# Kernel optimization log

Measured on AMD Instinct MI355X. Metric: run time of the kernel, lower is better.

## Reference

```python
import jax, jax.numpy as jnp
import numpy as np

D_IN = 1024
D_OUT = 1024
NUM_HEADS = 16
HEAD_DIM = D_OUT // NUM_HEADS


def setup_inputs() -> dict:
    key = jax.random.key(0)
    ks = jax.random.split(key, 4)
    B, T = 2, 2048
    x = jax.random.normal(ks[0], (B, T, D_IN), dtype=jnp.float32)
    # Linear(d_in, 3*d_out, bias=False): weight shape (3*d_out, d_in)
    w_qkv = jax.random.normal(ks[1], (3 * D_OUT, D_IN), dtype=jnp.float32) * (1.0 / np.sqrt(D_IN))
    # Linear(d_out, d_out) with bias
    w_out = jax.random.normal(ks[2], (D_OUT, D_OUT), dtype=jnp.float32) * (1.0 / np.sqrt(D_OUT))
    b_out = jax.random.normal(ks[3], (D_OUT,), dtype=jnp.float32) * 0.01
    return {"x": x, "w_qkv": w_qkv, "w_out": w_out, "b_out": b_out}


def reference(x, w_qkv, w_out, b_out):
    B, T, C = x.shape
    H, Dh = NUM_HEADS, HEAD_DIM
    qkv = jnp.einsum('btc,fc->btf', x, w_qkv)          # (B, T, 3*d_out)
    q, k, v = jnp.split(qkv, 3, axis=-1)
    # (B, H, T, Dh)
    q = q.reshape(B, T, H, Dh).transpose(0, 2, 1, 3)
    k = k.reshape(B, T, H, Dh).transpose(0, 2, 1, 3)
    v = v.reshape(B, T, H, Dh).transpose(0, 2, 1, 3)
    scale = 1.0 / np.sqrt(Dh).astype(np.float32)
    scores = jnp.einsum('bhqd,bhkd->bhqk', q, k) * scale
    causal = jnp.tril(jnp.ones((T, T), dtype=bool))    # True = keep
    scores = jnp.where(causal, scores, -jnp.inf)
    weights = jax.nn.softmax(scores, axis=-1)
    y = jnp.einsum('bhqk,bhkd->bhqd', weights, v)
    y = y.transpose(0, 2, 1, 3).reshape(B, T, C)
    return jnp.einsum('btc,oc->bto', y, w_out) + b_out
```

## Files before the change

kernel.cpp:

```cpp
#include <hip/hip_runtime.h>
#include <stdint.h>


typedef __bf16 bf16x8 __attribute__((ext_vector_type(8)));
typedef float  f32x4  __attribute__((ext_vector_type(4)));
typedef float  f32x16 __attribute__((ext_vector_type(16)));

#define MFMA16(a, b, c) __builtin_amdgcn_mfma_f32_16x16x32_bf16((a), (b), (c), 0, 0, 0)
#define MFMA32(a, b, c) __builtin_amdgcn_mfma_f32_32x32x16_bf16((a), (b), (c), 0, 0, 0)

__device__ __forceinline__ unsigned short f2bf(float f) {
    union { float f; unsigned int u; } c;
    c.f = f;
    unsigned int u = c.u;
    return (unsigned short)((u + 0x7fffu + ((u >> 16) & 1u)) >> 16);
}

__device__ __forceinline__ unsigned cvtpk(float lo, float hi) {
    unsigned r;
    asm("v_cvt_pk_bf16_f32 %0, %1, %2" : "=v"(r) : "v"(lo), "v"(hi));
    return r;
}

__global__ __launch_bounds__(256) void cvt3_kernel(const float* __restrict__ a,
                                                   const float* __restrict__ b,
                                                   const float* __restrict__ c,
                                                   unsigned short* __restrict__ out,
                                                   int na4, int nb4, int ntot4) {
    int i = blockIdx.x * 256 + threadIdx.x;
    const int stride = gridDim.x * 256;
    for (; i < ntot4; i += stride) {
        const float4* src;
        int j;
        if (i < na4)            { src = (const float4*)a; j = i; }
        else if (i < na4 + nb4) { src = (const float4*)b; j = i - na4; }
        else                    { src = (const float4*)c; j = i - na4 - nb4; }
        float4 v = src[j];
        ushort4 o;
        o.x = f2bf(v.x); o.y = f2bf(v.y); o.z = f2bf(v.z); o.w = f2bf(v.w);
        reinterpret_cast<ushort4*>(out)[i] = o;
    }
}

__device__ __forceinline__ void gload_lds16(const void* g, void* l) {
    __builtin_amdgcn_global_load_lds((const __attribute__((address_space(1))) void*)g,
                                     (__attribute__((address_space(3))) void*)l,
                                     16, 0, 0);
}

__device__ __forceinline__ void gemm_core_128(const unsigned short* __restrict__ A,
                                              const unsigned short* __restrict__ B,
                                              int K, int tM, int tN,
                                              unsigned short* As, unsigned short* Bs,
                                              f32x4 acc[4][4]) {
    const int tid  = threadIdx.x;
    const int lane = tid & 63;
    const int w    = tid >> 6;
    const int wr   = w >> 1, wc = w & 1;
    const int lr   = lane & 15, lg = lane >> 4;

    const int o0 = tid * 16;
    const int o1 = o0 + 4096;
    const int row0 = o0 >> 6, cb0 = o0 & 63;
    const int row1 = o1 >> 6, cb1 = o1 & 63;

    const char* Ab = (const char*)A;
    const char* Bb = (const char*)B;
    const size_t rstride = (size_t)K * 2;

    for (int kt = 0; kt < K; kt += 32) {
        const size_t kbyte = (size_t)kt * 2;
        gload_lds16(Ab + (size_t)(tM + row0) * rstride + kbyte + cb0, (char*)As + o0);
        gload_lds16(Ab + (size_t)(tM + row1) * rstride + kbyte + cb1, (char*)As + o1);
        gload_lds16(Bb + (size_t)(tN + row0) * rstride + kbyte + cb0, (char*)Bs + o0);
        gload_lds16(Bb + (size_t)(tN + row1) * rstride + kbyte + cb1, (char*)Bs + o1);
        __syncthreads();

        bf16x8 a[4], b[4];
#pragma unroll
        for (int m = 0; m < 4; ++m)
            a[m] = *reinterpret_cast<const bf16x8*>(As + (wr * 64 + m * 16 + lr) * 32 + lg * 8);
#pragma unroll
        for (int n = 0; n < 4; ++n)
            b[n] = *reinterpret_cast<const bf16x8*>(Bs + (wc * 64 + n * 16 + lr) * 32 + lg * 8);
#pragma unroll
        for (int m = 0; m < 4; ++m)
#pragma unroll
            for (int n = 0; n < 4; ++n)
                acc[m][n] = MFMA16(a[m], b[n], acc[m][n]);
        __syncthreads();
    }
}

__global__ __launch_bounds__(256) void gemm_qkv_kernel(const unsigned short* __restrict__ Xb,
                                                       const unsigned short* __restrict__ Wb,
                                                       unsigned short* __restrict__ Qo,
                                                       unsigned short* __restrict__ Ko,
                                                       unsigned short* __restrict__ Vt) {
    __shared__ __align__(16) unsigned short As[128 * 32];
    __shared__ __align__(16) unsigned short Bs[128 * 32];
    f32x4 acc[4][4];
#pragma unroll
    for (int m = 0; m < 4; ++m)
#pragma unroll
        for (int n = 0; n < 4; ++n)
#pragma unroll
            for (int r = 0; r < 4; ++r) acc[m][n][r] = 0.0f;

    const int wg = (blockIdx.x & 7) * 96 + (blockIdx.x >> 3);
    const int tM = (wg / 24) * 128;
    const int tN = (wg % 24) * 128;
    gemm_core_128(Xb, Wb, 1024, tM, tN, As, Bs, acc);

    const int lane = threadIdx.x & 63, w = threadIdx.x >> 6;
    const int wr = w >> 1, wc = w & 1, lr = lane & 15, lg = lane >> 4;
    const float QSCALE = 0.125f * 1.44269504088896340736f;
#pragma unroll
    for (int m = 0; m < 4; ++m)
#pragma unroll
        for (int n = 0; n < 4; ++n)
#pragma unroll
            for (int r = 0; r < 4; ++r) {
                const int gr = tM + wr * 64 + m * 16 + 4 * lg + r;
                const int gc = tN + wc * 64 + n * 16 + lr;
                const float v = acc[m][n][r];
                const int bb = gr >> 11, t = gr & 2047;
                const int kind = gc >> 10, c = gc & 1023;
                const int h = c >> 6, d = c & 63;
                const int bh = bb * 16 + h;
                if (kind == 0) {
                    Qo[((size_t)bh * 2048 + t) * 64 + d] = f2bf(v * QSCALE);
                } else if (kind == 1) {
                    const int off = ((t >> 5) << 11) + ((d >> 4) << 9) + ((t & 31) << 4) + (d & 15);
                    Ko[((size_t)bh << 17) + off] = f2bf(v);
                } else {
                    const int off = ((t >> 6) << 12) + ((d >> 5) << 11) + (((t >> 4) & 3) << 9)
                                  + ((d & 31) << 4) + (t & 15);
                    Vt[((size_t)bh << 17) + off] = f2bf(v);
                }
            }
}

__global__ __launch_bounds__(256) void gemm_out_kernel(const unsigned short* __restrict__ Yb,
                                                       const unsigned short* __restrict__ Wob,
                                                       const float* __restrict__ bias,
                                                       float* __restrict__ out) {
    __shared__ __align__(16) unsigned short As[128 * 32];
    __shared__ __align__(16) unsigned short Bs[64 * 32];
    const int tid = threadIdx.x, lane = tid & 63, w = tid >> 6;
    const int wr = w >> 1, wc = w & 1, lr = lane & 15, lg = lane >> 4;

    const int wg = (blockIdx.x & 7) * 64 + (blockIdx.x >> 3);
    const int tM = (wg >> 4) * 128;
    const int tN = (wg & 15) * 64;

    f32x4 acc[4][2];
#pragma unroll
    for (int m = 0; m < 4; ++m)
#pragma unroll
        for (int n = 0; n < 2; ++n)
#pragma unroll
            for (int r = 0; r < 4; ++r) acc[m][n][r] = 0.0f;

    const int o0 = tid * 16;
    const int o1 = o0 + 4096;
    const int rowA0 = o0 >> 6, cbA0 = o0 & 63;
    const int rowA1 = o1 >> 6, cbA1 = o1 & 63;
    const int rowB  = o0 >> 6, cbB  = o0 & 63;

    const char* Ab = (const char*)Yb;
    const char* Bb = (const char*)Wob;

    for (int kt = 0; kt < 1024; kt += 32) {
        const size_t kbyte = (size_t)kt * 2;
        gload_lds16(Ab + (size_t)(tM + rowA0) * 2048 + kbyte + cbA0, (char*)As + o0);
        gload_lds16(Ab + (size_t)(tM + rowA1) * 2048 + kbyte + cbA1, (char*)As + o1);
        gload_lds16(Bb + (size_t)(tN + rowB) * 2048 + kbyte + cbB, (char*)Bs + o0);
        __syncthreads();

        bf16x8 a[4], b[2];
#pragma unroll
        for (int m = 0; m < 4; ++m)
            a[m] = *reinterpret_cast<const bf16x8*>(As + (wr * 64 + m * 16 + lr) * 32 + lg * 8);
#pragma unroll
        for (int n = 0; n < 2; ++n)
            b[n] = *reinterpret_cast<const bf16x8*>(Bs + (wc * 32 + n * 16 + lr) * 32 + lg * 8);
#pragma unroll
        for (int m = 0; m < 4; ++m)
#pragma unroll
            for (int n = 0; n < 2; ++n)
                acc[m][n] = MFMA16(a[m], b[n], acc[m][n]);
        __syncthreads();
    }

#pragma unroll
    for (int m = 0; m < 4; ++m)
#pragma unroll
        for (int n = 0; n < 2; ++n)
#pragma unroll
            for (int r = 0; r < 4; ++r) {
                const int gr = tM + wr * 64 + m * 16 + 4 * lg + r;
                const int gc = tN + wc * 32 + n * 16 + lr;
                out[(size_t)gr * 1024 + gc] = acc[m][n][r] + bias[gc];
            }
}

__global__ __launch_bounds__(256, 2) void attn_kernel(const unsigned short* __restrict__ Q,
                                                      const unsigned short* __restrict__ Kb,
                                                      const unsigned short* __restrict__ Vt,
                                                      unsigned short* __restrict__ Y) {
    __shared__ __align__(16) float4 part[3][64][9];
    const int tid = threadIdx.x, lane = tid & 63, w = tid >> 6;
    const int l31 = lane & 31, hi = lane >> 5;
    const int fo  = (l31 << 4) + (hi << 3);

    const int bid = blockIdx.x;
    const int wg  = (bid & 7) * 256 + (bid >> 3);
    const int bh  = wg >> 6;
    const int qt  = 63 - (wg & 63);
    const int qw  = qt * 32;

    const unsigned short* Qh = Q  + (size_t)bh * 2048 * 64;
    const unsigned short* Kh = Kb + ((size_t)bh << 17);
    const unsigned short* Vh = Vt + ((size_t)bh << 17);

    bf16x8 qf[4];
#pragma unroll
    for (int c = 0; c < 4; ++c)
        qf[c] = *reinterpret_cast<const bf16x8*>(Qh + (size_t)(qw + l31) * 64 + c * 16 + hi * 8);

    f32x16 o0, o1;
#pragma unroll
    for (int r = 0; r < 16; ++r) { o0[r] = 0.0f; o1[r] = 0.0f; }
    float lrun = 0.0f;

    const int qg  = qw + l31;
    const int n64 = (qw >> 6) + 1;

    union UB { unsigned u[4]; bf16x8 v; };
#define PACK_HALF(SV, base, OUT) {                                        \
        unsigned lo01 = cvtpk(SV[(base) + 0], SV[(base) + 1]);            \
        unsigned lo23 = cvtpk(SV[(base) + 2], SV[(base) + 3]);            \
        unsigned hi01 = cvtpk(SV[(base) + 4], SV[(base) + 5]);            \
        unsigned hi23 = cvtpk(SV[(base) + 6], SV[(base) + 7]);            \
        unsigned s01  = hi ? lo01 : hi01;                                 \
        unsigned s23  = hi ? lo23 : hi23;                                 \
        unsigned r01  = __shfl_xor(s01, 32, 64);                          \
        unsigned r23  = __shfl_xor(s23, 32, 64);                          \
        OUT.u[0] = hi ? r01  : lo01;                                      \
        OUT.u[1] = hi ? r23  : lo23;                                      \
        OUT.u[2] = hi ? hi01 : r01;                                       \
        OUT.u[3] = hi ? hi23 : r23; }

    for (int j = w; j < n64; j += 4) {
        const int kb = j << 6;
        const bool act1 = (kb + 32 <= qw + 31);

        const unsigned short* Kt = Kh + ((size_t)(kb >> 5) << 11);
        const unsigned short* Vb = Vh + ((size_t)(kb >> 6) << 12);
        bf16x8 kf0[4], kf1[4], vf0[4], vf1[4];
#pragma unroll
        for (int c = 0; c < 4; ++c)
            kf0[c] = *reinterpret_cast<const bf16x8*>(Kt + (c << 9) + fo);
        if (act1) {
#pragma unroll
            for (int c = 0; c < 4; ++c)
                kf1[c] = *reinterpret_cast<const bf16x8*>(Kt + 2048 + (c << 9) + fo);
        }
#pragma unroll
        for (int c = 0; c < 4; ++c) {
            vf0[c] = *reinterpret_cast<const bf16x8*>(Vb + (c << 9) + fo);
            vf1[c] = *reinterpret_cast<const bf16x8*>(Vb + 2048 + (c << 9) + fo);
        }

        f32x16 s0, s1;
#pragma unroll
        for (int r = 0; r < 16; ++r) { s0[r] = 0.0f; s1[r] = 0.0f; }
#pragma unroll
        for (int c = 0; c < 4; ++c) s0 = MFMA32(kf0[c], qf[c], s0);
        if (act1) {
#pragma unroll
            for (int c = 0; c < 4; ++c) s1 = MFMA32(kf1[c], qf[c], s1);
        }

        if (kb + 31 > qw) {
#pragma unroll
            for (int r = 0; r < 16; ++r) {
                const int kv = kb + (r & 3) + 8 * (r >> 2) + 4 * hi;
                s0[r] = (kv > qg) ? -INFINITY : s0[r];
            }
        }
        if (kb + 63 > qw) {
#pragma unroll
            for (int r = 0; r < 16; ++r) {
                const int kv = kb + 32 + (r & 3) + 8 * (r >> 2) + 4 * hi;
                s1[r] = (kv > qg) ? -INFINITY : s1[r];
            }
        }

#pragma unroll
        for (int r = 0; r < 16; ++r) {
            s0[r] = __builtin_amdgcn_exp2f(s0[r]);
            s1[r] = __builtin_amdgcn_exp2f(s1[r]);
        }

        float u8[8];
#pragma unroll
        for (int r = 0; r < 8; ++r)
            u8[r] = (s0[r] + s0[r + 8]) + (s1[r] + s1[r + 8]);
        float us = ((u8[0] + u8[1]) + (u8[2] + u8[3])) + ((u8[4] + u8[5]) + (u8[6] + u8[7]));
        us += __shfl_xor(us, 32, 64);
        lrun += us;

        UB p0, p1, p2, p3;
        PACK_HALF(s0, 0, p0); PACK_HALF(s0, 8, p1);
        PACK_HALF(s1, 0, p2); PACK_HALF(s1, 8, p3);

        o0 = MFMA32(vf0[0], p0.v, o0);
        o0 = MFMA32(vf0[1], p1.v, o0);
        o0 = MFMA32(vf0[2], p2.v, o0);
        o0 = MFMA32(vf0[3], p3.v, o0);
        o1 = MFMA32(vf1[0], p0.v, o1);
        o1 = MFMA32(vf1[1], p1.v, o1);
        o1 = MFMA32(vf1[2], p2.v, o1);
        o1 = MFMA32(vf1[3], p3.v, o1);
    }
#undef PACK_HALF

    if (w) {
        float4* row = &part[w - 1][lane][0];
#pragma unroll
        for (int q4 = 0; q4 < 4; ++q4)
            row[q4] = make_float4(o0[q4 * 4], o0[q4 * 4 + 1], o0[q4 * 4 + 2], o0[q4 * 4 + 3]);
#pragma unroll
        for (int q4 = 0; q4 < 4; ++q4)
            row[4 + q4] = make_float4(o1[q4 * 4], o1[q4 * 4 + 1], o1[q4 * 4 + 2], o1[q4 * 4 + 3]);
        row[8] = make_float4(lrun, 0.0f, 0.0f, 0.0f);
    }
    __syncthreads();
    if (w == 0) {
#pragma unroll
        for (int wv = 0; wv < 3; ++wv) {
            const float4* row = &part[wv][lane][0];
#pragma unroll
            for (int q4 = 0; q4 < 4; ++q4) {
                float4 a = row[q4], b = row[4 + q4];
                o0[q4 * 4] += a.x; o0[q4 * 4 + 1] += a.y; o0[q4 * 4 + 2] += a.z; o0[q4 * 4 + 3] += a.w;
                o1[q4 * 4] += b.x; o1[q4 * 4 + 1] += b.y; o1[q4 * 4 + 2] += b.z; o1[q4 * 4 + 3] += b.w;
            }
            lrun += row[8].x;
        }

        const float inv = 1.0f / lrun;
        const int bb = bh >> 4, hh = bh & 15;
        unsigned short* Yrow = Y + ((size_t)(bb * 2048 + qg)) * 1024 + hh * 64;
#pragma unroll
        for (int r = 0; r < 16; ++r) {
            const int d = (r & 3) + 8 * (r >> 2) + 4 * hi;
            Yrow[d]      = f2bf(o0[r] * inv);
            Yrow[32 + d] = f2bf(o1[r] * inv);
        }
    }
}

extern "C" void kernel_launch(void* const* d_in, const int* in_sizes, int n_in,
                              void* d_out, int out_size, void* d_ws, size_t ws_size,
                              hipStream_t stream) {
    (void)in_sizes; (void)n_in; (void)out_size; (void)ws_size;
    const float* x     = (const float*)d_in[0];
    const float* w_qkv = (const float*)d_in[1];
    const float* w_out = (const float*)d_in[2];
    const float* b_out = (const float*)d_in[3];
    float* out = (float*)d_out;

    unsigned short* xb    = (unsigned short*)d_ws;
    unsigned short* Yb    = xb;
    unsigned short* wqkvb = xb    + (size_t)4096 * 1024;
    unsigned short* woutb = wqkvb + (size_t)3072 * 1024;
    unsigned short* Qb    = woutb + (size_t)1024 * 1024;
    unsigned short* Kbuf  = Qb    + (size_t)32 * 2048 * 64;
    unsigned short* Vt    = Kbuf  + (size_t)32 * 2048 * 64;

    const int na4 = 4096 * 1024 / 4, nb4 = 3072 * 1024 / 4, nc4 = 1024 * 1024 / 4;
    cvt3_kernel<<<2048, 256, 0, stream>>>(x, w_qkv, w_out, xb, na4, nb4, na4 + nb4 + nc4);
    gemm_qkv_kernel<<<768, 256, 0, stream>>>(xb, wqkvb, Qb, Kbuf, Vt);
    attn_kernel<<<2048, 256, 0, stream>>>(Qb, Kbuf, Vt, Yb);
    gemm_out_kernel<<<512, 256, 0, stream>>>(Yb, woutb, b_out, out);
}
```

Before: 172.0 us.

## Triple-buffer LDS staging in QKV and output projection GEMMs

Replaces the single-buffered load/sync/compute loops in both projection GEMMs with a 3-stage ring of LDS buffers. Loads for tile i+2 are issued while tile i is computed, and a partial vmcnt wait plus one barrier per iteration replace the two __syncthreads. This is meant to hide global-load latency behind MFMA work. In exchange it triples LDS use per block, which could reduce occupancy, and it relies on hand-written waitcnt counts staying correct.

```diff
diff --git a/kernel.cpp b/kernel.cpp
--- a/kernel.cpp
+++ b/kernel.cpp
@@ -48,72 +48,69 @@
                                      16, 0, 0);
 }
 
-__device__ __forceinline__ void gemm_core_128(const unsigned short* __restrict__ A,
-                                              const unsigned short* __restrict__ B,
-                                              int K, int tM, int tN,
-                                              unsigned short* As, unsigned short* Bs,
-                                              f32x4 acc[4][4]) {
-    const int tid  = threadIdx.x;
-    const int lane = tid & 63;
-    const int w    = tid >> 6;
-    const int wr   = w >> 1, wc = w & 1;
-    const int lr   = lane & 15, lg = lane >> 4;
-
-    const int o0 = tid * 16;
-    const int o1 = o0 + 4096;
-    const int row0 = o0 >> 6, cb0 = o0 & 63;
-    const int row1 = o1 >> 6, cb1 = o1 & 63;
-
-    const char* Ab = (const char*)A;
-    const char* Bb = (const char*)B;
-    const size_t rstride = (size_t)K * 2;
-
-    for (int kt = 0; kt < K; kt += 32) {
-        const size_t kbyte = (size_t)kt * 2;
-        gload_lds16(Ab + (size_t)(tM + row0) * rstride + kbyte + cb0, (char*)As + o0);
-        gload_lds16(Ab + (size_t)(tM + row1) * rstride + kbyte + cb1, (char*)As + o1);
-        gload_lds16(Bb + (size_t)(tN + row0) * rstride + kbyte + cb0, (char*)Bs + o0);
-        gload_lds16(Bb + (size_t)(tN + row1) * rstride + kbyte + cb1, (char*)Bs + o1);
-        __syncthreads();
-
-        bf16x8 a[4], b[4];
-#pragma unroll
-        for (int m = 0; m < 4; ++m)
-            a[m] = *reinterpret_cast<const bf16x8*>(As + (wr * 64 + m * 16 + lr) * 32 + lg * 8);
-#pragma unroll
-        for (int n = 0; n < 4; ++n)
-            b[n] = *reinterpret_cast<const bf16x8*>(Bs + (wc * 64 + n * 16 + lr) * 32 + lg * 8);
-#pragma unroll
-        for (int m = 0; m < 4; ++m)
-#pragma unroll
-            for (int n = 0; n < 4; ++n)
-                acc[m][n] = MFMA16(a[m], b[n], acc[m][n]);
-        __syncthreads();
-    }
-}
-
 __global__ __launch_bounds__(256) void gemm_qkv_kernel(const unsigned short* __restrict__ Xb,
                                                        const unsigned short* __restrict__ Wb,
                                                        unsigned short* __restrict__ Qo,
                                                        unsigned short* __restrict__ Ko,
                                                        unsigned short* __restrict__ Vt) {
-    __shared__ __align__(16) unsigned short As[128 * 32];
-    __shared__ __align__(16) unsigned short Bs[128 * 32];
-    f32x4 acc[4][4];
-#pragma unroll
-    for (int m = 0; m < 4; ++m)
-#pragma unroll
-        for (int n = 0; n < 4; ++n)
-#pragma unroll
-            for (int r = 0; r < 4; ++r) acc[m][n][r] = 0.0f;
+    __shared__ __align__(16) unsigned short As[3 * 4096];
+    __shared__ __align__(16) unsigned short Bs[3 * 4096];
+    const int tid = threadIdx.x, lane = tid & 63, w = tid >> 6;
+    const int wr = w >> 1, wc = w & 1, lr = lane & 15, lg = lane >> 4;
 
     const int wg = (blockIdx.x & 7) * 96 + (blockIdx.x >> 3);
     const int tM = (wg / 24) * 128;
     const int tN = (wg % 24) * 128;
-    gemm_core_128(Xb, Wb, 1024, tM, tN, As, Bs, acc);
-
-    const int lane = threadIdx.x & 63, w = threadIdx.x >> 6;
-    const int wr = w >> 1, wc = w & 1, lr = lane & 15, lg = lane >> 4;
+
+    f32x4 acc[4][4];
+#pragma unroll
+    for (int m = 0; m < 4; ++m)
+#pragma unroll
+        for (int n = 0; n < 4; ++n)
+#pragma unroll
+            for (int r = 0; r < 4; ++r) acc[m][n][r] = 0.0f;
+
+    const int o0 = tid * 16, o1 = o0 + 4096;
+    const int row0 = o0 >> 6, cb0 = o0 & 63;
+    const int row1 = o1 >> 6, cb1 = o1 & 63;
+    const char* Ab = (const char*)Xb;
+    const char* Bb = (const char*)Wb;
+
+#define STAGE_Q(bi, kt) { const size_t kb_ = (size_t)(kt) * 2;                                 \
+        gload_lds16(Ab + (size_t)(tM + row0) * 2048 + kb_ + cb0, (char*)As + (bi) * 8192 + o0); \
+        gload_lds16(Ab + (size_t)(tM + row1) * 2048 + kb_ + cb1, (char*)As + (bi) * 8192 + o1); \
+        gload_lds16(Bb + (size_t)(tN + row0) * 2048 + kb_ + cb0, (char*)Bs + (bi) * 8192 + o0); \
+        gload_lds16(Bb + (size_t)(tN + row1) * 2048 + kb_ + cb1, (char*)Bs + (bi) * 8192 + o1); }
+
+    STAGE_Q(0, 0);
+    STAGE_Q(1, 32);
+    for (int i = 0; i < 32; ++i) {
+        __builtin_amdgcn_sched_barrier(0);
+        if (i < 31) asm volatile("s_waitcnt vmcnt(4) lgkmcnt(0)" ::: "memory");
+        else        asm volatile("s_waitcnt vmcnt(0) lgkmcnt(0)" ::: "memory");
+        __builtin_amdgcn_sched_barrier(0);
+        __builtin_amdgcn_s_barrier();
+        __builtin_amdgcn_sched_barrier(0);
+        const int bi = i % 3;
+        if (i + 2 < 32) STAGE_Q((i + 2) % 3, (i + 2) * 32);
+
+        const unsigned short* Av = As + bi * 4096;
+        const unsigned short* Bv = Bs + bi * 4096;
+        bf16x8 a[4], b[4];
+#pragma unroll
+        for (int m = 0; m < 4; ++m)
+            a[m] = *reinterpret_cast<const bf16x8*>(Av + (wr * 64 + m * 16 + lr) * 32 + lg * 8);
+#pragma unroll
+        for (int n = 0; n < 4; ++n)
+            b[n] = *reinterpret_cast<const bf16x8*>(Bv + (wc * 64 + n * 16 + lr) * 32 + lg * 8);
+#pragma unroll
+        for (int m = 0; m < 4; ++m)
+#pragma unroll
+            for (int n = 0; n < 4; ++n)
+                acc[m][n] = MFMA16(a[m], b[n], acc[m][n]);
+    }
+#undef STAGE_Q
+
     const float QSCALE = 0.125f * 1.44269504088896340736f;
 #pragma unroll
     for (int m = 0; m < 4; ++m)
@@ -145,8 +142,8 @@
                                                        const unsigned short* __restrict__ Wob,
                                                        const float* __restrict__ bias,
                                                        float* __restrict__ out) {
-    __shared__ __align__(16) unsigned short As[128 * 32];
-    __shared__ __align__(16) unsigned short Bs[64 * 32];
+    __shared__ __align__(16) unsigned short As[3 * 4096];
+    __shared__ __align__(16) unsigned short Bs[3 * 2048];
     const int tid = threadIdx.x, lane = tid & 63, w = tid >> 6;
     const int wr = w >> 1, wc = w & 1, lr = lane & 15, lg = lane >> 4;
 
@@ -162,36 +159,46 @@
 #pragma unroll
             for (int r = 0; r < 4; ++r) acc[m][n][r] = 0.0f;
 
-    const int o0 = tid * 16;
-    const int o1 = o0 + 4096;
+    const int o0 = tid * 16, o1 = o0 + 4096;
     const int rowA0 = o0 >> 6, cbA0 = o0 & 63;
     const int rowA1 = o1 >> 6, cbA1 = o1 & 63;
-    const int rowB  = o0 >> 6, cbB  = o0 & 63;
-
+    const int rowB = o0 >> 6, cbB = o0 & 63;
     const char* Ab = (const char*)Yb;
     const char* Bb = (const char*)Wob;
 
-    for (int kt = 0; kt < 1024; kt += 32) {
-        const size_t kbyte = (size_t)kt * 2;
-        gload_lds16(Ab + (size_t)(tM + rowA0) * 2048 + kbyte + cbA0, (char*)As + o0);
-        gload_lds16(Ab + (size_t)(tM + rowA1) * 2048 + kbyte + cbA1, (char*)As + o1);
-        gload_lds16(Bb + (size_t)(tN + rowB) * 2048 + kbyte + cbB, (char*)Bs + o0);
-        __syncthreads();
-
+#define STAGE_O(bi, kt) { const size_t kb_ = (size_t)(kt) * 2;                                   \
+        gload_lds16(Ab + (size_t)(tM + rowA0) * 2048 + kb_ + cbA0, (char*)As + (bi) * 8192 + o0); \
+        gload_lds16(Ab + (size_t)(tM + rowA1) * 2048 + kb_ + cbA1, (char*)As + (bi) * 8192 + o1); \
+        gload_lds16(Bb + (size_t)(tN + rowB) * 2048 + kb_ + cbB, (char*)Bs + (bi) * 4096 + o0); }
+
+    STAGE_O(0, 0);
+    STAGE_O(1, 32);
+    for (int i = 0; i < 32; ++i) {
+        __builtin_amdgcn_sched_barrier(0);
+        if (i < 31) asm volatile("s_waitcnt vmcnt(3) lgkmcnt(0)" ::: "memory");
+        else        asm volatile("s_waitcnt vmcnt(0) lgkmcnt(0)" ::: "memory");
+        __builtin_amdgcn_sched_barrier(0);
+        __builtin_amdgcn_s_barrier();
+        __builtin_amdgcn_sched_barrier(0);
+        const int bi = i % 3;
+        if (i + 2 < 32) STAGE_O((i + 2) % 3, (i + 2) * 32);
+
+        const unsigned short* Av = As + bi * 4096;
+        const unsigned short* Bv = Bs + bi * 2048;
         bf16x8 a[4], b[2];
 #pragma unroll
         for (int m = 0; m < 4; ++m)
-            a[m] = *reinterpret_cast<const bf16x8*>(As + (wr * 64 + m * 16 + lr) * 32 + lg * 8);
+            a[m] = *reinterpret_cast<const bf16x8*>(Av + (wr * 64 + m * 16 + lr) * 32 + lg * 8);
 #pragma unroll
         for (int n = 0; n < 2; ++n)
-            b[n] = *reinterpret_cast<const bf16x8*>(Bs + (wc * 32 + n * 16 + lr) * 32 + lg * 8);
+            b[n] = *reinterpret_cast<const bf16x8*>(Bv + (wc * 32 + n * 16 + lr) * 32 + lg * 8);
 #pragma unroll
         for (int m = 0; m < 4; ++m)
 #pragma unroll
             for (int n = 0; n < 2; ++n)
                 acc[m][n] = MFMA16(a[m], b[n], acc[m][n]);
-        __syncthreads();
-    }
+    }
+#undef STAGE_O
 
 #pragma unroll
     for (int m = 0; m < 4; ++m)
```

Result: no change. 173.7 us (+1.0%).
